# Performance work log

Hardware: AMD Instinct MI355X
Metric: run time of the kernel (lower is better)

Reference implementation:

```python
import jax, jax.numpy as jnp
import numpy as np

SPARSITY_RATIO = 0.5

def setup_inputs() -> dict:
    key = jax.random.key(0)
    x = jax.random.normal(key, (32, 128, 128, 128), dtype=jnp.float32)
    return {"x": x}

def reference(x) -> jnp.ndarray:
    B, C, H, W = x.shape
    k = int(SPARSITY_RATIO * H * W)
    absx = jnp.abs(x)
    flat = absx.reshape(B, C, H * W)
    # k-th largest |x| per (b, c) is the threshold
    topvals = jax.lax.top_k(flat, k)[0]          # [B, C, k]
    thresh = topvals[:, :, -1][:, :, None, None]  # [B, C, 1, 1]
    comp = (absx >= thresh).astype(x.dtype)
    return comp * x
```

## Files before the change

kernel.cpp:

```cpp
#include <hip/hip_runtime.h>

#define THREADS 512
#define HW 16384
#define K_SEL 8192u
#define NB1 2048
#define NB2 1024
#define NB3 1024
#define VPT 8

static_assert(THREADS * VPT * 4 == HW, "row tiling");

template <int NBINS>
__device__ __forceinline__ void find_bin_wave0(const unsigned* __restrict__ hist,
                                               unsigned kRem, unsigned* __restrict__ bc) {
  constexpr int bpl = NBINS >> 6;
  const int lane = (int)(threadIdx.x & 63);
  const int base = lane * bpl;
  unsigned s = 0;
#pragma unroll
  for (int j = 0; j < bpl; ++j) s += hist[base + ((j + lane) & (bpl - 1))];
  unsigned suf = s;
#pragma unroll
  for (int off = 1; off < 64; off <<= 1) {
    unsigned w = __shfl_down(suf, off);
    if (lane + off < 64) suf += w;
  }
  const unsigned cumAbove = suf - s;
  const bool hit = (cumAbove < kRem) && (kRem <= suf);
  const unsigned long long m = __ballot(hit);
  const int tl = (int)__builtin_ctzll(m);
  const unsigned cumTl = __shfl(cumAbove, tl);
  const int j = lane & (bpl - 1);
  const unsigned h = hist[tl * bpl + j];
  unsigned sufc = h;
#pragma unroll
  for (int off = 1; off < 32; off <<= 1) {
    if (off < bpl) {
      unsigned w = __shfl_down(sufc, off);
      if (j + off < bpl) sufc += w;
    }
  }
  const unsigned cumW = sufc - h;
  const bool hit2 = ((cumTl + cumW) < kRem) && (kRem <= cumTl + cumW + h);
  const unsigned long long m2 = __ballot(hit2);
  const int jl = (int)__builtin_ctzll(m2) & (bpl - 1);
  const unsigned kw = __shfl(cumW, jl);
  if (lane == 0) {
    bc[0] = (unsigned)(tl * bpl + jl);
    bc[1] = kRem - cumTl - kw;
  }
}

extern "C" __global__ __launch_bounds__(THREADS, 8)
void sparsify_topk_kernel(const float* __restrict__ x, float* __restrict__ out) {
  __shared__ unsigned h1[NB1];
  __shared__ unsigned h2[NB2];
  __shared__ unsigned h3[NB3];
  __shared__ unsigned bc[2];

  const int t = (int)threadIdx.x;
  const size_t rowOff = (size_t)blockIdx.x * (HW / 4);
  const uint4* src = (const uint4*)x + rowOff;
  uint4*       dst = (uint4*)out + rowOff;

  uint4 v[VPT];
#pragma unroll
  for (int i = 0; i < VPT; ++i) v[i] = src[i * THREADS + t];

#pragma unroll
  for (int i = 0; i < NB1 / THREADS; ++i) h1[t + i * THREADS] = 0;
#pragma unroll
  for (int i = 0; i < NB2 / THREADS; ++i) h2[t + i * THREADS] = 0;
#pragma unroll
  for (int i = 0; i < NB3 / THREADS; ++i) h3[t + i * THREADS] = 0;
  __syncthreads();

#pragma unroll
  for (int i = 0; i < VPT; ++i) {
    atomicAdd(&h1[(v[i].x & 0x7fffffffu) >> 20], 1u);
    atomicAdd(&h1[(v[i].y & 0x7fffffffu) >> 20], 1u);
    atomicAdd(&h1[(v[i].z & 0x7fffffffu) >> 20], 1u);
    atomicAdd(&h1[(v[i].w & 0x7fffffffu) >> 20], 1u);
  }
  __syncthreads();
  if (t < 64) find_bin_wave0<NB1>(h1, K_SEL, bc);
  __syncthreads();
  const unsigned T1 = bc[0];
  unsigned kRem = bc[1];

#pragma unroll
  for (int i = 0; i < VPT; ++i) {
    unsigned a;
    a = v[i].x & 0x7fffffffu; if ((a >> 20) == T1) atomicAdd(&h2[(a >> 10) & (NB2 - 1)], 1u);
    a = v[i].y & 0x7fffffffu; if ((a >> 20) == T1) atomicAdd(&h2[(a >> 10) & (NB2 - 1)], 1u);
    a = v[i].z & 0x7fffffffu; if ((a >> 20) == T1) atomicAdd(&h2[(a >> 10) & (NB2 - 1)], 1u);
    a = v[i].w & 0x7fffffffu; if ((a >> 20) == T1) atomicAdd(&h2[(a >> 10) & (NB2 - 1)], 1u);
  }
  __syncthreads();
  if (t < 64) find_bin_wave0<NB2>(h2, kRem, bc);
  __syncthreads();
  const unsigned pref2 = (T1 << 10) | bc[0];
  kRem = bc[1];

#pragma unroll
  for (int i = 0; i < VPT; ++i) {
    unsigned a;
    a = v[i].x & 0x7fffffffu; if ((a >> 10) == pref2) atomicAdd(&h3[a & (NB3 - 1)], 1u);
    a = v[i].y & 0x7fffffffu; if ((a >> 10) == pref2) atomicAdd(&h3[a & (NB3 - 1)], 1u);
    a = v[i].z & 0x7fffffffu; if ((a >> 10) == pref2) atomicAdd(&h3[a & (NB3 - 1)], 1u);
    a = v[i].w & 0x7fffffffu; if ((a >> 10) == pref2) atomicAdd(&h3[a & (NB3 - 1)], 1u);
  }
  __syncthreads();
  if (t < 64) find_bin_wave0<NB3>(h3, kRem, bc);
  __syncthreads();
  const unsigned thr = (pref2 << 10) | bc[0];

#pragma unroll
  for (int i = 0; i < VPT; ++i) {
    uint4 w = v[i];
    w.x = ((w.x & 0x7fffffffu) >= thr) ? w.x : 0u;
    w.y = ((w.y & 0x7fffffffu) >= thr) ? w.y : 0u;
    w.z = ((w.z & 0x7fffffffu) >= thr) ? w.z : 0u;
    w.w = ((w.w & 0x7fffffffu) >= thr) ? w.w : 0u;
    dst[i * THREADS + t] = w;
  }
}

extern "C" void kernel_launch(void* const* d_in, const int* in_sizes, int n_in,
                              void* d_out, int out_size, void* d_ws, size_t ws_size,
                              hipStream_t stream) {
  (void)n_in; (void)d_ws; (void)ws_size; (void)out_size;
  const float* x = (const float*)d_in[0];
  float* out = (float*)d_out;
  const int rows = in_sizes[0] / HW;
  sparsify_topk_kernel<<<dim3(rows), dim3(THREADS), 0, stream>>>(x, out);
}
```

Before: 115.2 us.

## Compact pass-2 candidates into LDS list and use nontemporal output stores

During the second histogram pass, elements that fall in the selected top bin are appended to a shared-memory candidate list. The third pass then scans only that list instead of all 32 register values per thread, and falls back to the full scan if the list overflows. Output stores become nontemporal to avoid polluting the cache. The cost is an extra LDS atomic per candidate in pass 2, 12KB more LDS that may reduce occupancy, and contention on a single counter.

```diff
diff --git a/kernel.cpp b/kernel.cpp
--- a/kernel.cpp
+++ b/kernel.cpp
@@ -7,8 +7,11 @@
 #define NB2 1024
 #define NB3 1024
 #define VPT 8
+#define CAP 3072
 
 static_assert(THREADS * VPT * 4 == HW, "row tiling");
+
+typedef unsigned uint32x4 __attribute__((ext_vector_type(4)));
 
 template <int NBINS>
 __device__ __forceinline__ void find_bin_wave0(const unsigned* __restrict__ hist,
@@ -56,12 +59,14 @@
   __shared__ unsigned h1[NB1];
   __shared__ unsigned h2[NB2];
   __shared__ unsigned h3[NB3];
+  __shared__ unsigned list[CAP];
   __shared__ unsigned bc[2];
+  __shared__ unsigned cnt;
 
   const int t = (int)threadIdx.x;
   const size_t rowOff = (size_t)blockIdx.x * (HW / 4);
   const uint4* src = (const uint4*)x + rowOff;
-  uint4*       dst = (uint4*)out + rowOff;
+  uint32x4*    dst = (uint32x4*)out + rowOff;
 
   uint4 v[VPT];
 #pragma unroll
@@ -73,6 +78,7 @@
   for (int i = 0; i < NB2 / THREADS; ++i) h2[t + i * THREADS] = 0;
 #pragma unroll
   for (int i = 0; i < NB3 / THREADS; ++i) h3[t + i * THREADS] = 0;
+  if (t == 0) cnt = 0;
   __syncthreads();
 
 #pragma unroll
@@ -91,24 +97,37 @@
 #pragma unroll
   for (int i = 0; i < VPT; ++i) {
     unsigned a;
-    a = v[i].x & 0x7fffffffu; if ((a >> 20) == T1) atomicAdd(&h2[(a >> 10) & (NB2 - 1)], 1u);
-    a = v[i].y & 0x7fffffffu; if ((a >> 20) == T1) atomicAdd(&h2[(a >> 10) & (NB2 - 1)], 1u);
-    a = v[i].z & 0x7fffffffu; if ((a >> 20) == T1) atomicAdd(&h2[(a >> 10) & (NB2 - 1)], 1u);
-    a = v[i].w & 0x7fffffffu; if ((a >> 20) == T1) atomicAdd(&h2[(a >> 10) & (NB2 - 1)], 1u);
+#define P2_ONE(comp)                                                        \
+    a = v[i].comp & 0x7fffffffu;                                            \
+    if ((a >> 20) == T1) {                                                  \
+      atomicAdd(&h2[(a >> 10) & (NB2 - 1)], 1u);                            \
+      const unsigned idx = atomicAdd(&cnt, 1u);                             \
+      if (idx < CAP) list[idx] = a;                                         \
+    }
+    P2_ONE(x) P2_ONE(y) P2_ONE(z) P2_ONE(w)
+#undef P2_ONE
   }
   __syncthreads();
   if (t < 64) find_bin_wave0<NB2>(h2, kRem, bc);
   __syncthreads();
   const unsigned pref2 = (T1 << 10) | bc[0];
   kRem = bc[1];
+  const unsigned nCand = cnt;
 
+  if (nCand <= CAP) {
+    for (unsigned i = t; i < nCand; i += THREADS) {
+      const unsigned a = list[i];
+      if ((a >> 10) == pref2) atomicAdd(&h3[a & (NB3 - 1)], 1u);
+    }
+  } else {
 #pragma unroll
-  for (int i = 0; i < VPT; ++i) {
-    unsigned a;
-    a = v[i].x & 0x7fffffffu; if ((a >> 10) == pref2) atomicAdd(&h3[a & (NB3 - 1)], 1u);
-    a = v[i].y & 0x7fffffffu; if ((a >> 10) == pref2) atomicAdd(&h3[a & (NB3 - 1)], 1u);
-    a = v[i].z & 0x7fffffffu; if ((a >> 10) == pref2) atomicAdd(&h3[a & (NB3 - 1)], 1u);
-    a = v[i].w & 0x7fffffffu; if ((a >> 10) == pref2) atomicAdd(&h3[a & (NB3 - 1)], 1u);
+    for (int i = 0; i < VPT; ++i) {
+      unsigned a;
+      a = v[i].x & 0x7fffffffu; if ((a >> 10) == pref2) atomicAdd(&h3[a & (NB3 - 1)], 1u);
+      a = v[i].y & 0x7fffffffu; if ((a >> 10) == pref2) atomicAdd(&h3[a & (NB3 - 1)], 1u);
+      a = v[i].z & 0x7fffffffu; if ((a >> 10) == pref2) atomicAdd(&h3[a & (NB3 - 1)], 1u);
+      a = v[i].w & 0x7fffffffu; if ((a >> 10) == pref2) atomicAdd(&h3[a & (NB3 - 1)], 1u);
+    }
   }
   __syncthreads();
   if (t < 64) find_bin_wave0<NB3>(h3, kRem, bc);
@@ -117,12 +136,13 @@
 
 #pragma unroll
   for (int i = 0; i < VPT; ++i) {
-    uint4 w = v[i];
-    w.x = ((w.x & 0x7fffffffu) >= thr) ? w.x : 0u;
-    w.y = ((w.y & 0x7fffffffu) >= thr) ? w.y : 0u;
-    w.z = ((w.z & 0x7fffffffu) >= thr) ? w.z : 0u;
-    w.w = ((w.w & 0x7fffffffu) >= thr) ? w.w : 0u;
-    dst[i * THREADS + t] = w;
+    const uint4 w = v[i];
+    uint32x4 o;
+    o.x = ((w.x & 0x7fffffffu) >= thr) ? w.x : 0u;
+    o.y = ((w.y & 0x7fffffffu) >= thr) ? w.y : 0u;
+    o.z = ((w.z & 0x7fffffffu) >= thr) ? w.z : 0u;
+    o.w = ((w.w & 0x7fffffffu) >= thr) ? w.w : 0u;
+    __builtin_nontemporal_store(o, &dst[i * THREADS + t]);
   }
 }
 
```

Result: slower. 189.0 us (+64.1%).
